# Optimization experiments

Hardware: AMD Instinct MI355X
Metric: run time of the kernel (lower is better)

Reference implementation:

```python
import jax, jax.numpy as jnp
import numpy as np

# norse LIF parameters from the module: LIFParameters(tau_syn_inv=400, tau_mem_inv=200)
# remaining norse defaults: dt=1e-3, v_th=1.0, v_leak=0.0, v_reset=0.0, SuperSpike alpha=100
DT = 1e-3
TAU_SYN_INV = 400.0
TAU_MEM_INV = 200.0
V_TH = 1.0
ALPHA = 100.0


@jax.custom_vjp
def heaviside(x):
    return (x > 0).astype(x.dtype)


def _heaviside_fwd(x):
    return heaviside(x), x


def _heaviside_bwd(x, g):
    # SuperSpike surrogate gradient: 1 / (alpha*|x| + 1)^2
    return (g / (ALPHA * jnp.abs(x) + 1.0) ** 2,)


heaviside.defvjp(_heaviside_fwd, _heaviside_bwd)


def lif_step(inp, v, i):
    # explicit-Euler LIF update (norse lif_feed_forward_step)
    v_decayed = v + DT * TAU_MEM_INV * (i - v)          # v_leak = 0
    i_decayed = i + DT * TAU_SYN_INV * (-i)
    z = heaviside(v_decayed - V_TH)
    v_new = (1.0 - z) * v_decayed                        # v_reset = 0
    i_new = i_decayed + inp
    return z, v_new, i_new


def setup_inputs() -> dict:
    key = jax.random.key(0)
    T, B, H, W = 256, 16, 128, 128
    x = jax.random.normal(key, (T, B, H, W), dtype=jnp.float32)
    return {"x": x}


def reference(x):
    # x: [T, B, H, W]. Two stacked feed-forward LIF cells (module calls l1 twice)
    # with independent states, scanned over time.
    zeros = jnp.zeros(x.shape[1:], x.dtype)

    def step(carry, xt):
        v1, i1, v2, i2 = carry
        z1, v1, i1 = lif_step(xt, v1, i1)
        z2, v2, i2 = lif_step(z1, v2, i2)
        return (v1, i1, v2, i2), z2

    _, out = jax.lax.scan(step, (zeros, zeros, zeros, zeros), x)
    return out  # [T, B, H, W]
```

## Files before the change

kernel.cpp:

```cpp
#include <hip/hip_runtime.h>

#define VM_K 0.2f
#define SYN_DECAY 0.6f
#define V_TH 1.0f

__global__ __launch_bounds__(256) void lif_scan_kernel(
    const float4* __restrict__ x, float4* __restrict__ out, int N4, int T)
{
    int idx = blockIdx.x * blockDim.x + threadIdx.x;
    if (idx >= N4) return;

    float4 v1 = make_float4(0.f, 0.f, 0.f, 0.f);
    float4 i1 = v1, v2 = v1, i2 = v1;

    const float4* xp = x + idx;
    float4* op = out + idx;

#pragma unroll 4
    for (int t = 0; t < T; ++t) {
        float4 xt = xp[(size_t)t * N4];
        float4 z2;

        {
            float v1d = v1.x + VM_K * (i1.x - v1.x);
            float z1  = (v1d - V_TH > 0.f) ? 1.f : 0.f;
            v1.x = (1.f - z1) * v1d;
            i1.x = SYN_DECAY * i1.x + xt.x;
            float v2d = v2.x + VM_K * (i2.x - v2.x);
            float z2c = (v2d - V_TH > 0.f) ? 1.f : 0.f;
            v2.x = (1.f - z2c) * v2d;
            i2.x = SYN_DECAY * i2.x + z1;
            z2.x = z2c;
        }
        {
            float v1d = v1.y + VM_K * (i1.y - v1.y);
            float z1  = (v1d - V_TH > 0.f) ? 1.f : 0.f;
            v1.y = (1.f - z1) * v1d;
            i1.y = SYN_DECAY * i1.y + xt.y;
            float v2d = v2.y + VM_K * (i2.y - v2.y);
            float z2c = (v2d - V_TH > 0.f) ? 1.f : 0.f;
            v2.y = (1.f - z2c) * v2d;
            i2.y = SYN_DECAY * i2.y + z1;
            z2.y = z2c;
        }
        {
            float v1d = v1.z + VM_K * (i1.z - v1.z);
            float z1  = (v1d - V_TH > 0.f) ? 1.f : 0.f;
            v1.z = (1.f - z1) * v1d;
            i1.z = SYN_DECAY * i1.z + xt.z;
            float v2d = v2.z + VM_K * (i2.z - v2.z);
            float z2c = (v2d - V_TH > 0.f) ? 1.f : 0.f;
            v2.z = (1.f - z2c) * v2d;
            i2.z = SYN_DECAY * i2.z + z1;
            z2.z = z2c;
        }
        {
            float v1d = v1.w + VM_K * (i1.w - v1.w);
            float z1  = (v1d - V_TH > 0.f) ? 1.f : 0.f;
            v1.w = (1.f - z1) * v1d;
            i1.w = SYN_DECAY * i1.w + xt.w;
            float v2d = v2.w + VM_K * (i2.w - v2.w);
            float z2c = (v2d - V_TH > 0.f) ? 1.f : 0.f;
            v2.w = (1.f - z2c) * v2d;
            i2.w = SYN_DECAY * i2.w + z1;
            z2.w = z2c;
        }

        op[(size_t)t * N4] = z2;
    }
}

extern "C" void kernel_launch(void* const* d_in, const int* in_sizes, int n_in,
                              void* d_out, int out_size, void* d_ws, size_t ws_size,
                              hipStream_t stream) {
    const float* x = (const float*)d_in[0];
    float* out = (float*)d_out;

    const int T = 256;
    const int N = in_sizes[0] / T;
    const int N4 = N / 4;

    const int block = 256;
    const int grid = (N4 + block - 1) / block;

    lif_scan_kernel<<<grid, block, 0, stream>>>(
        (const float4*)x, (float4*)out, N4, T);
}
```

Baseline: 96.83 us.

## Use one scalar neuron per thread with nontemporal loads and stores

New measurement: 98.40 us. About the same (+1.6%).

```diff
diff --git a/kernel.cpp b/kernel.cpp
--- a/kernel.cpp
+++ b/kernel.cpp
@@ -2,71 +2,33 @@
 
 #define VM_K 0.2f
 #define SYN_DECAY 0.6f
-#define V_TH 1.0f
 
 __global__ __launch_bounds__(256) void lif_scan_kernel(
-    const float4* __restrict__ x, float4* __restrict__ out, int N4, int T)
+    const float* __restrict__ x, float* __restrict__ out, int N, int T)
 {
     int idx = blockIdx.x * blockDim.x + threadIdx.x;
-    if (idx >= N4) return;
+    if (idx >= N) return;
 
-    float4 v1 = make_float4(0.f, 0.f, 0.f, 0.f);
-    float4 i1 = v1, v2 = v1, i2 = v1;
+    float v1 = 0.f, i1 = 0.f, v2 = 0.f, i2 = 0.f;
 
-    const float4* xp = x + idx;
-    float4* op = out + idx;
+    const float* xp = x + idx;
+    float* op = out + idx;
 
-#pragma unroll 4
+#pragma unroll 8
     for (int t = 0; t < T; ++t) {
-        float4 xt = xp[(size_t)t * N4];
-        float4 z2;
+        float xt = __builtin_nontemporal_load(&xp[(size_t)t * N]);
 
-        {
-            float v1d = v1.x + VM_K * (i1.x - v1.x);
-            float z1  = (v1d - V_TH > 0.f) ? 1.f : 0.f;
-            v1.x = (1.f - z1) * v1d;
-            i1.x = SYN_DECAY * i1.x + xt.x;
-            float v2d = v2.x + VM_K * (i2.x - v2.x);
-            float z2c = (v2d - V_TH > 0.f) ? 1.f : 0.f;
-            v2.x = (1.f - z2c) * v2d;
-            i2.x = SYN_DECAY * i2.x + z1;
-            z2.x = z2c;
-        }
-        {
-            float v1d = v1.y + VM_K * (i1.y - v1.y);
-            float z1  = (v1d - V_TH > 0.f) ? 1.f : 0.f;
-            v1.y = (1.f - z1) * v1d;
-            i1.y = SYN_DECAY * i1.y + xt.y;
-            float v2d = v2.y + VM_K * (i2.y - v2.y);
-            float z2c = (v2d - V_TH > 0.f) ? 1.f : 0.f;
-            v2.y = (1.f - z2c) * v2d;
-            i2.y = SYN_DECAY * i2.y + z1;
-            z2.y = z2c;
-        }
-        {
-            float v1d = v1.z + VM_K * (i1.z - v1.z);
-            float z1  = (v1d - V_TH > 0.f) ? 1.f : 0.f;
-            v1.z = (1.f - z1) * v1d;
-            i1.z = SYN_DECAY * i1.z + xt.z;
-            float v2d = v2.z + VM_K * (i2.z - v2.z);
-            float z2c = (v2d - V_TH > 0.f) ? 1.f : 0.f;
-            v2.z = (1.f - z2c) * v2d;
-            i2.z = SYN_DECAY * i2.z + z1;
-            z2.z = z2c;
-        }
-        {
-            float v1d = v1.w + VM_K * (i1.w - v1.w);
-            float z1  = (v1d - V_TH > 0.f) ? 1.f : 0.f;
-            v1.w = (1.f - z1) * v1d;
-            i1.w = SYN_DECAY * i1.w + xt.w;
-            float v2d = v2.w + VM_K * (i2.w - v2.w);
-            float z2c = (v2d - V_TH > 0.f) ? 1.f : 0.f;
-            v2.w = (1.f - z2c) * v2d;
-            i2.w = SYN_DECAY * i2.w + z1;
-            z2.w = z2c;
-        }
+        float v1d = v1 + VM_K * (i1 - v1);
+        float z1  = (v1d > 1.0f) ? 1.f : 0.f;
+        v1 = (v1d > 1.0f) ? 0.f : v1d;
+        i1 = SYN_DECAY * i1 + xt;
 
-        op[(size_t)t * N4] = z2;
+        float v2d = v2 + VM_K * (i2 - v2);
+        float z2  = (v2d > 1.0f) ? 1.f : 0.f;
+        v2 = (v2d > 1.0f) ? 0.f : v2d;
+        i2 = SYN_DECAY * i2 + z1;
+
+        __builtin_nontemporal_store(z2, &op[(size_t)t * N]);
     }
 }
 
@@ -78,11 +40,9 @@
 
     const int T = 256;
     const int N = in_sizes[0] / T;
-    const int N4 = N / 4;
 
     const int block = 256;
-    const int grid = (N4 + block - 1) / block;
+    const int grid = (N + block - 1) / block;
 
-    lif_scan_kernel<<<grid, block, 0, stream>>>(
-        (const float4*)x, (float4*)out, N4, T);
+    lif_scan_kernel<<<grid, block, 0, stream>>>(x, out, N, T);
 }
```
